# Kernel optimization log

Measured on AMD Instinct MI355X. Metric: run time of the kernel, lower is better.

## Reference

```python
import jax, jax.numpy as jnp
import numpy as np

B, S, D, H = 2, 2048, 1024, 16
DH = D // H  # dim per head (dim_singl_head)
SCALE = 0.02


def layer_norm(x, g, b, eps=1e-5):
    m = jnp.mean(x, axis=-1, keepdims=True)
    v = jnp.mean((x - m) ** 2, axis=-1, keepdims=True)
    return (x - m) / jnp.sqrt(v + eps) * g + b


def setup_inputs() -> dict:
    key = jax.random.key(0)
    ks = jax.random.split(key, 12)
    return {
        "query": jax.random.normal(ks[0], (B, S, D), jnp.float32),
        "key": jax.random.normal(ks[1], (B, S, D), jnp.float32),
        "value": jax.random.normal(ks[2], (B, S, D), jnp.float32),
        "mask": jax.random.randint(ks[3], (B, S), 0, 2).astype(jnp.int32),
        "Wq": jax.random.normal(ks[4], (D, D), jnp.float32) * SCALE,
        "bq": jnp.zeros((D,), jnp.float32),
        "Wk": jax.random.normal(ks[5], (D, D), jnp.float32) * SCALE,
        "bk": jnp.zeros((D,), jnp.float32),
        "Wv": jax.random.normal(ks[6], (D, D), jnp.float32) * SCALE,
        "bv": jnp.zeros((D,), jnp.float32),
        "g_att": jnp.ones((DH,), jnp.float32),
        "b_att": jnp.zeros((DH,), jnp.float32),
        "Wres": jax.random.normal(ks[7], (D, D), jnp.float32) * SCALE,
        "bres": jnp.zeros((D,), jnp.float32),
        "g_out": jnp.ones((D,), jnp.float32),
        "b_out": jnp.zeros((D,), jnp.float32),
    }


def reference(query, key, value, mask, Wq, bq, Wk, bk, Wv, bv,
              g_att, b_att, Wres, bres, g_out, b_out):
    # split heads: torch's split(dh,-1)+cat(dim=0) == [H,B,S,dh] layout
    def heads(x):
        return x.reshape(B, S, H, DH).transpose(2, 0, 1, 3)  # [H,B,S,dh]

    q = heads(query @ Wq + bq)
    k = heads(key @ Wk + bk)
    v = heads(value @ Wv + bv)

    # additive mask: (1-mask)*-1e9, broadcast [1,B,1,Sk]
    madd = (1.0 - mask.astype(q.dtype))[None, :, None, :] * -1e9

    scores = jnp.einsum('hbqd,hbkd->hbqk', q, k) / np.float32(np.sqrt(DH))
    w = jax.nn.softmax(scores + madd, axis=-1)
    out = jnp.einsum('hbqk,hbkd->hbqd', w, v)

    out = out + q                         # residual_att
    out = layer_norm(out, g_att, b_att)   # per-head LayerNorm on dh

    # concat heads back: [H,B,S,dh] -> [B,S,H*dh]
    out = out.transpose(1, 2, 0, 3).reshape(B, S, D)

    out = out + jnp.tanh(out @ Wres + bres)  # residual_out branch
    out = layer_norm(out, g_out, b_out)      # norm_out
    return jnp.tanh(out)                     # final activation
```

## Files before the change

### kernel.cpp

```cpp
#include <hip/hip_runtime.h>
#include <cstdint>
#include <cstddef>

#define BB 2
#define SS 2048
#define DD 1024
#define HH 16
#define DHH 64
#define MROWS (BB*SS)

typedef short short8 __attribute__((ext_vector_type(8)));
typedef short short4v __attribute__((ext_vector_type(4)));
typedef float floatx4 __attribute__((ext_vector_type(4)));
typedef unsigned int uint2v __attribute__((ext_vector_type(2)));

#define GAS __attribute__((address_space(1)))
#define LAS __attribute__((address_space(3)))

__device__ __forceinline__ float4 ld4(const float* p) { return *(const float4*)p; }

__device__ __forceinline__ short f2bf(float x) {
    unsigned u = __builtin_bit_cast(unsigned, x);
    unsigned r = (u + 0x7fffu + ((u >> 16) & 1u)) >> 16;
    return (short)r;
}

__device__ __forceinline__ unsigned cvtpk(float lo, float hi) {
    unsigned r;
    asm("v_cvt_pk_bf16_f32 %0, %1, %2" : "=v"(r) : "v"(lo), "v"(hi));
    return r;
}

__device__ __forceinline__ void gl_lds16(const short* g, short* l) {
    __builtin_amdgcn_global_load_lds((const GAS unsigned int*)g,
                                     (LAS unsigned int*)l, 16, 0, 0);
}

__global__ __launch_bounds__(256) void convert_kernel(
    const float* __restrict__ s0, const float* __restrict__ s1, const float* __restrict__ s2,
    short* __restrict__ d0, short* __restrict__ d1, short* __restrict__ d2)
{
    const float* s; short* d;
    if (blockIdx.z == 0)      { s = s0; d = d0; }
    else if (blockIdx.z == 1) { s = s1; d = d1; }
    else                      { s = s2; d = d2; }
    size_t idx = ((size_t)blockIdx.x * 256 + threadIdx.x) * 8;
    float4 a = ld4(s + idx);
    float4 b = ld4(s + idx + 4);
    short8 p;
    p[0] = f2bf(a.x); p[1] = f2bf(a.y); p[2] = f2bf(a.z); p[3] = f2bf(a.w);
    p[4] = f2bf(b.x); p[5] = f2bf(b.y); p[6] = f2bf(b.z); p[7] = f2bf(b.w);
    *(short8*)(d + idx) = p;
}

__global__ __launch_bounds__(256) void transpose_w_kernel(
    const float* __restrict__ W0, const float* __restrict__ W1,
    const float* __restrict__ W2, const float* __restrict__ W3,
    short* __restrict__ T0, short* __restrict__ T1,
    short* __restrict__ T2, short* __restrict__ T3)
{
    const float* W; short* T;
    if (blockIdx.z == 0)      { W = W0; T = T0; }
    else if (blockIdx.z == 1) { W = W1; T = T1; }
    else if (blockIdx.z == 2) { W = W2; T = T2; }
    else                      { W = W3; T = T3; }

    __shared__ short tile[64 * 72];
    const int t  = threadIdx.x;
    const int k0 = blockIdx.x * 64, n0 = blockIdx.y * 64;
#pragma unroll
    for (int i = 0; i < 4; i++) {
        int flat = i * 256 + t;
        int row = flat >> 4;
        int c4  = (flat & 15) * 4;
        float4 v = ld4(W + (size_t)(k0 + row) * DD + n0 + c4);
        tile[(c4 + 0) * 72 + row] = f2bf(v.x);
        tile[(c4 + 1) * 72 + row] = f2bf(v.y);
        tile[(c4 + 2) * 72 + row] = f2bf(v.z);
        tile[(c4 + 3) * 72 + row] = f2bf(v.w);
    }
    __syncthreads();
#pragma unroll
    for (int i = 0; i < 4; i++) {
        int flat = i * 256 + t;
        int nrow = flat >> 4;
        int kc   = (flat & 15) * 4;
        short4v pk = *(short4v*)&tile[nrow * 72 + kc];
        *(short4v*)(T + (size_t)(n0 + nrow) * DD + k0 + kc) = pk;
    }
}

__global__ __launch_bounds__(256) void gemm_bf16_kernel(
    const short* __restrict__ A0, const short* __restrict__ A1, const short* __restrict__ A2,
    const short* __restrict__ Bt0, const short* __restrict__ Bt1, const short* __restrict__ Bt2,
    const float* __restrict__ b0, const float* __restrict__ b1, const float* __restrict__ b2,
    float* __restrict__ Cf0, float* __restrict__ Cf1, float* __restrict__ Cf2,
    short* __restrict__ Cb0, short* __restrict__ Cb1, short* __restrict__ Cb2,
    short* __restrict__ Ct0, short* __restrict__ Ct1, short* __restrict__ Ct2,
    float cs0, float cs1, float cs2)
{
    const short* A; const short* Bt; const float* bias;
    float* Cf; short* Cb; short* Ct; float cbs;
    if (blockIdx.z == 0)      { A = A0; Bt = Bt0; bias = b0; Cf = Cf0; Cb = Cb0; Ct = Ct0; cbs = cs0; }
    else if (blockIdx.z == 1) { A = A1; Bt = Bt1; bias = b1; Cf = Cf1; Cb = Cb1; Ct = Ct1; cbs = cs1; }
    else                      { A = A2; Bt = Bt2; bias = b2; Cf = Cf2; Cb = Cb2; Ct = Ct2; cbs = cs2; }

    __shared__ __align__(16) short As[128 * 32];
    __shared__ __align__(16) short Bs[128 * 32];

    const int tid  = threadIdx.x;
    const int lane = tid & 63;
    const int wave = tid >> 6;
    const int quad = lane >> 4;
    const int l15  = lane & 15;
    const int m0 = blockIdx.y * 128;
    const int n0 = blockIdx.x * 128;
    const int wr = (wave >> 1) * 64;
    const int wc = (wave & 1) * 64;

    floatx4 acc[4][4];
#pragma unroll
    for (int mt = 0; mt < 4; mt++)
#pragma unroll
        for (int nt = 0; nt < 4; nt++) acc[mt][nt] = (floatx4)0.0f;

    for (int k0 = 0; k0 < DD; k0 += 32) {
        __syncthreads();
#pragma unroll
        for (int j = 0; j < 2; j++) {
            int chunk = j * 256 + tid;
            int row = chunk >> 2;
            int ch  = chunk & 3;
            gl_lds16(A  + (size_t)(m0 + row) * DD + k0 + ch * 8, &As[chunk * 8]);
            gl_lds16(Bt + (size_t)(n0 + row) * DD + k0 + ch * 8, &Bs[chunk * 8]);
        }
        __syncthreads();

        short8 af[4], bf[4];
#pragma unroll
        for (int mt = 0; mt < 4; mt++)
            af[mt] = *(const short8*)&As[(wr + mt * 16 + l15) * 32 + quad * 8];
#pragma unroll
        for (int nt = 0; nt < 4; nt++)
            bf[nt] = *(const short8*)&Bs[(wc + nt * 16 + l15) * 32 + quad * 8];
#pragma unroll
        for (int mt = 0; mt < 4; mt++)
#pragma unroll
            for (int nt = 0; nt < 4; nt++)
                acc[mt][nt] = __builtin_amdgcn_mfma_f32_16x16x32_bf16(af[mt], bf[nt], acc[mt][nt], 0, 0, 0);
    }

    float biasv[4];
#pragma unroll
    for (int nt = 0; nt < 4; nt++) biasv[nt] = bias[n0 + wc + nt * 16 + l15];

    if (Cf || Cb) {
#pragma unroll
        for (int mt = 0; mt < 4; mt++)
#pragma unroll
            for (int r = 0; r < 4; r++) {
                const int m = m0 + wr + mt * 16 + quad * 4 + r;
                const size_t rowb = (size_t)m * DD + n0 + wc;
#pragma unroll
                for (int nt = 0; nt < 4; nt++) {
                    float v = acc[mt][nt][r] + biasv[nt];
                    if (Cf) Cf[rowb + nt * 16 + l15] = v;
                    if (Cb) Cb[rowb + nt * 16 + l15] = f2bf(v * cbs);
                }
            }
    }
    if (Ct) {
#pragma unroll
        for (int mt = 0; mt < 4; mt++) {
            const int mbase = m0 + wr + mt * 16 + quad * 4;
            const int bb = mbase >> 11;
            const int s0 = mbase & 2047;
#pragma unroll
            for (int nt = 0; nt < 4; nt++) {
                const int c = n0 + wc + nt * 16 + l15;
                short4v pk;
#pragma unroll
                for (int r = 0; r < 4; r++) pk[r] = f2bf(acc[mt][nt][r] + biasv[nt]);
                *(short4v*)(Ct + ((size_t)(bb * 1024 + c)) * SS + s0) = pk;
            }
        }
    }
}

__global__ __launch_bounds__(256, 2) void attn_mfma_kernel(
    const short* __restrict__ Qb, const short* __restrict__ Kb, const short* __restrict__ Vt,
    const float* __restrict__ Qf, const int* __restrict__ mask,
    const float* __restrict__ g_att, const float* __restrict__ b_att,
    float* __restrict__ X, short* __restrict__ Xb)
{
    const int tid  = threadIdx.x;
    const int lane = tid & 63;
    const int wave = tid >> 6;
    const int quad = lane >> 4;
    const int l15  = lane & 15;

    const int h  = blockIdx.y;
    const int b  = blockIdx.z;
    const int q0 = blockIdx.x * 128;
    const int bS = b * SS;

    __shared__ __align__(16) short Ks[2 * 64 * 72];
    __shared__ __align__(16) short Vs[2 * 64 * 72];
    __shared__ __align__(16) short Ps[4 * 32 * 68];
    __shared__ float smadd[2 * 64];

    short8 qf[2][2];
#pragma unroll
    for (int mt = 0; mt < 2; mt++)
#pragma unroll
        for (int s = 0; s < 2; s++)
            qf[mt][s] = *(const short8*)(Qb +
                (size_t)(bS + q0 + wave * 32 + mt * 16 + l15) * DD + h * 64 + s * 32 + quad * 8);

    floatx4 o[2][4];
#pragma unroll
    for (int mt = 0; mt < 2; mt++)
#pragma unroll
        for (int nt = 0; nt < 4; nt++) o[mt][nt] = (floatx4)0.0f;
    float lsum[2] = {0.0f, 0.0f};

    const int srow = tid >> 3;
    const int sch  = tid & 7;

    short8 kreg[2], vreg[2];
    float mreg;
    {
#pragma unroll
        for (int i = 0; i < 2; i++) {
            int row = srow + i * 32;
            kreg[i] = *(const short8*)(Kb + (size_t)(bS + row) * DD + h * 64 + sch * 8);
            vreg[i] = *(const short8*)(Vt + (size_t)(b * 1024 + h * 64 + row) * SS + sch * 8);
        }
        mreg = (tid < 64) ? (float)mask[bS + tid] : 0.0f;
    }

    for (int kt = 0; kt < SS / 64; kt++) {
        const int bufo = (kt & 1) * (64 * 72);
#pragma unroll
        for (int i = 0; i < 2; i++) {
            int row = srow + i * 32;
            *(short8*)&Ks[bufo + row * 72 + sch * 8] = kreg[i];
            *(short8*)&Vs[bufo + row * 72 + sch * 8] = vreg[i];
        }
        if (tid < 64) smadd[(kt & 1) * 64 + tid] = (1.0f - mreg) * -1e9f;

        if (kt < SS / 64 - 1) {
            const int k0n = (kt + 1) * 64;
#pragma unroll
            for (int i = 0; i < 2; i++) {
                int row = srow + i * 32;
                kreg[i] = *(const short8*)(Kb + (size_t)(bS + k0n + row) * DD + h * 64 + sch * 8);
                vreg[i] = *(const short8*)(Vt + (size_t)(b * 1024 + h * 64 + row) * SS + k0n + sch * 8);
            }
            mreg = (tid < 64) ? (float)mask[bS + k0n + tid] : 0.0f;
        }

        __builtin_amdgcn_s_waitcnt(0xC07F);
        __builtin_amdgcn_s_barrier();

#pragma unroll
        for (int nt = 0; nt < 4; nt++) {
            const float4 mrow = *(const float4*)&smadd[(kt & 1) * 64 + nt * 16 + quad * 4];
#pragma unroll
            for (int mt = 0; mt < 2; mt++) {
                floatx4 acc = (floatx4)0.0f;
#pragma unroll
                for (int s = 0; s < 2; s++) {
                    short8 kf = *(const short8*)&Ks[bufo + (nt * 16 + l15) * 72 + s * 32 + quad * 8];
                    acc = __builtin_amdgcn_mfma_f32_16x16x32_bf16(kf, qf[mt][s], acc, 0, 0, 0);
                }
                float p0 = __builtin_exp2f(acc[0] + mrow.x);
                float p1 = __builtin_exp2f(acc[1] + mrow.y);
                float p2 = __builtin_exp2f(acc[2] + mrow.z);
                float p3 = __builtin_exp2f(acc[3] + mrow.w);
                lsum[mt] += (p0 + p1) + (p2 + p3);
                unsigned w0 = cvtpk(p0, p1);
                unsigned w1 = cvtpk(p2, p3);
                *(uint2v*)&Ps[wave * 2176 + (mt * 16 + l15) * 68 + nt * 16 + quad * 4]
                    = (uint2v){w0, w1};
            }
        }

#pragma unroll
        for (int s = 0; s < 2; s++) {
            short8 pa[2];
#pragma unroll
            for (int mt = 0; mt < 2; mt++)
                pa[mt] = *(const short8*)&Ps[wave * 2176 + (mt * 16 + l15) * 68 + s * 32 + quad * 8];
#pragma unroll
            for (int nt = 0; nt < 4; nt++) {
                short8 vb = *(const short8*)&Vs[bufo + (nt * 16 + l15) * 72 + s * 32 + quad * 8];
#pragma unroll
                for (int mt = 0; mt < 2; mt++)
                    o[mt][nt] = __builtin_amdgcn_mfma_f32_16x16x32_bf16(pa[mt], vb, o[mt][nt], 0, 0, 0);
            }
        }
    }

#pragma unroll
    for (int mt = 0; mt < 2; mt++) {
        lsum[mt] += __shfl_xor(lsum[mt], 16);
        lsum[mt] += __shfl_xor(lsum[mt], 32);
    }
    float rlq[2][4];
#pragma unroll
    for (int mt = 0; mt < 2; mt++)
#pragma unroll
        for (int r = 0; r < 4; r++)
            rlq[mt][r] = 1.0f / __shfl(lsum[mt], (lane & 48) | (quad * 4 + r));

    float gvv[4], bvv[4];
#pragma unroll
    for (int nt = 0; nt < 4; nt++) { gvv[nt] = g_att[nt * 16 + l15]; bvv[nt] = b_att[nt * 16 + l15]; }

#pragma unroll
    for (int mt = 0; mt < 2; mt++) {
        float x[4][4];
        float sum[4] = {0.f, 0.f, 0.f, 0.f};
#pragma unroll
        for (int r = 0; r < 4; r++) {
            const float rl = rlq[mt][r];
            const int row = q0 + wave * 32 + mt * 16 + quad * 4 + r;
            const size_t base = (size_t)(bS + row) * DD + h * 64;
#pragma unroll
            for (int nt = 0; nt < 4; nt++) {
                float xv = o[mt][nt][r] * rl + Qf[base + nt * 16 + l15];
                x[nt][r] = xv;
                sum[r] += xv;
            }
        }
#pragma unroll
        for (int r = 0; r < 4; r++)
#pragma unroll
            for (int off = 1; off < 16; off <<= 1) sum[r] += __shfl_xor(sum[r], off);

        float vsum[4] = {0.f, 0.f, 0.f, 0.f}, mu[4];
#pragma unroll
        for (int r = 0; r < 4; r++) {
            mu[r] = sum[r] * (1.0f / 64.0f);
#pragma unroll
            for (int nt = 0; nt < 4; nt++) { float d = x[nt][r] - mu[r]; vsum[r] += d * d; }
        }
#pragma unroll
        for (int r = 0; r < 4; r++) {
#pragma unroll
            for (int off = 1; off < 16; off <<= 1) vsum[r] += __shfl_xor(vsum[r], off);
            float rstd = rsqrtf(vsum[r] * (1.0f / 64.0f) + 1e-5f);
            const int row = q0 + wave * 32 + mt * 16 + quad * 4 + r;
            const size_t base = (size_t)(bS + row) * DD + h * 64;
#pragma unroll
            for (int nt = 0; nt < 4; nt++) {
                float yv = (x[nt][r] - mu[r]) * rstd * gvv[nt] + bvv[nt];
                X[base + nt * 16 + l15] = yv;
                Xb[base + nt * 16 + l15] = f2bf(yv);
            }
        }
    }
}

__global__ __launch_bounds__(256) void lnout_kernel(
    const float* __restrict__ X, const float* __restrict__ Y,
    const float* __restrict__ g, const float* __restrict__ bcoef,
    float* __restrict__ out)
{
    const int r = blockIdx.x;
    const int t = threadIdx.x;
    const size_t base = (size_t)r * DD + (t << 2);
    float4 x = ld4(X + base);
    float4 y = ld4(Y + base);
    float4 z;
    z.x = x.x + tanhf(y.x);
    z.y = x.y + tanhf(y.y);
    z.z = x.z + tanhf(y.z);
    z.w = x.w + tanhf(y.w);

    __shared__ float red[4];
    __shared__ float stats[2];
    const int w = t >> 6;

    float sv = z.x + z.y + z.z + z.w;
#pragma unroll
    for (int off = 32; off > 0; off >>= 1) sv += __shfl_down(sv, off);
    if ((t & 63) == 0) red[w] = sv;
    __syncthreads();
    if (t == 0) stats[0] = (red[0] + red[1] + red[2] + red[3]) * (1.0f / 1024.0f);
    __syncthreads();
    const float mu = stats[0];

    float4 d;
    d.x = z.x - mu; d.y = z.y - mu; d.z = z.z - mu; d.w = z.w - mu;
    float s2 = d.x * d.x + d.y * d.y + d.z * d.z + d.w * d.w;
#pragma unroll
    for (int off = 32; off > 0; off >>= 1) s2 += __shfl_down(s2, off);
    if ((t & 63) == 0) red[w] = s2;
    __syncthreads();
    if (t == 0) stats[1] = rsqrtf((red[0] + red[1] + red[2] + red[3]) * (1.0f / 1024.0f) + 1e-5f);
    __syncthreads();
    const float rstd = stats[1];

    float4 gv = ld4(g + (t << 2));
    float4 bv = ld4(bcoef + (t << 2));
    float4 o;
    o.x = tanhf(d.x * rstd * gv.x + bv.x);
    o.y = tanhf(d.y * rstd * gv.y + bv.y);
    o.z = tanhf(d.z * rstd * gv.z + bv.z);
    o.w = tanhf(d.w * rstd * gv.w + bv.w);
    *(float4*)(out + base) = o;
}

extern "C" void kernel_launch(void* const* d_in, const int* in_sizes, int n_in,
                              void* d_out, int out_size, void* d_ws, size_t ws_size,
                              hipStream_t stream)
{
    const float* query = (const float*)d_in[0];
    const float* key   = (const float*)d_in[1];
    const float* value = (const float*)d_in[2];
    const int*   mask  = (const int*)  d_in[3];
    const float* Wq    = (const float*)d_in[4];
    const float* bq    = (const float*)d_in[5];
    const float* Wk    = (const float*)d_in[6];
    const float* bk    = (const float*)d_in[7];
    const float* Wv    = (const float*)d_in[8];
    const float* bv    = (const float*)d_in[9];
    const float* g_att = (const float*)d_in[10];
    const float* b_att = (const float*)d_in[11];
    const float* Wres  = (const float*)d_in[12];
    const float* bres  = (const float*)d_in[13];
    const float* g_out = (const float*)d_in[14];
    const float* b_out = (const float*)d_in[15];

    const size_t MAT = (size_t)MROWS * DD;
    float* fws = (float*)d_ws;
    float* Qw = fws;
    float* Xw = fws + MAT;
    short* Qb = (short*)(fws + 2 * MAT);
    short* Kb = Qb + MAT;
    short* Vt = Kb + MAT;
    short* qbf = Vt + MAT;
    short* kbf = qbf + MAT;
    short* vbf = kbf + MAT;
    short* Wtq = vbf + MAT;
    short* Wtk = Wtq + DD * DD;
    short* Wtv = Wtk + DD * DD;
    short* Wtr = Wtv + DD * DD;
    short* Xb = qbf;
    float* Yw = (float*)kbf;

    convert_kernel<<<dim3(MAT / 2048, 1, 3), 256, 0, stream>>>(
        query, key, value, qbf, kbf, vbf);

    transpose_w_kernel<<<dim3(16, 16, 4), 256, 0, stream>>>(
        Wq, Wk, Wv, Wres, Wtq, Wtk, Wtv, Wtr);

    gemm_bf16_kernel<<<dim3(8, 32, 3), 256, 0, stream>>>(
        qbf, kbf, vbf, Wtq, Wtk, Wtv, bq, bk, bv,
        Qw, nullptr, nullptr,
        Qb, Kb, nullptr,
        nullptr, nullptr, Vt,
        0.180336884f, 1.0f, 1.0f);

    attn_mfma_kernel<<<dim3(SS / 128, HH, BB), 256, 0, stream>>>(
        Qb, Kb, Vt, Qw, mask, g_att, b_att, Xw, Xb);

    gemm_bf16_kernel<<<dim3(8, 32, 1), 256, 0, stream>>>(
        Xb, Xb, Xb, Wtr, Wtr, Wtr, bres, bres, bres,
        Yw, Yw, Yw, nullptr, nullptr, nullptr, nullptr, nullptr, nullptr,
        1.0f, 1.0f, 1.0f);

    lnout_kernel<<<MROWS, 256, 0, stream>>>(Xw, Yw, g_out, b_out, (float*)d_out);
}
```

Measured before the change: 290.0 us.

## Split attention block across 8 waves of 16 query rows each

The attention kernel now launches 512 threads per block, and each wave handles 16 query rows instead of 32. The per-wave Q fragments, output accumulators and P staging buffer shrink, and each thread loads one K/V row chunk per tile instead of two. This is meant to raise wave-level parallelism and latency hiding and to cut register pressure, with a launch bound of 4 blocks per CU. In exchange, each K/V tile held in shared memory is reused by fewer rows per wave, and there are more waves taking part in every barrier.

```diff
diff --git a/kernel.cpp b/kernel.cpp
--- a/kernel.cpp
+++ b/kernel.cpp
@@ -187,7 +187,7 @@
     }
 }
 
-__global__ __launch_bounds__(256, 2) void attn_mfma_kernel(
+__global__ __launch_bounds__(512, 4) void attn_mfma_kernel(
     const short* __restrict__ Qb, const short* __restrict__ Kb, const short* __restrict__ Vt,
     const float* __restrict__ Qf, const int* __restrict__ mask,
     const float* __restrict__ g_att, const float* __restrict__ b_att,
@@ -206,57 +206,41 @@
 
     __shared__ __align__(16) short Ks[2 * 64 * 72];
     __shared__ __align__(16) short Vs[2 * 64 * 72];
-    __shared__ __align__(16) short Ps[4 * 32 * 68];
+    __shared__ __align__(16) short Ps[8 * 16 * 68];
     __shared__ float smadd[2 * 64];
 
-    short8 qf[2][2];
-#pragma unroll
-    for (int mt = 0; mt < 2; mt++)
-#pragma unroll
-        for (int s = 0; s < 2; s++)
-            qf[mt][s] = *(const short8*)(Qb +
-                (size_t)(bS + q0 + wave * 32 + mt * 16 + l15) * DD + h * 64 + s * 32 + quad * 8);
-
-    floatx4 o[2][4];
-#pragma unroll
-    for (int mt = 0; mt < 2; mt++)
-#pragma unroll
-        for (int nt = 0; nt < 4; nt++) o[mt][nt] = (floatx4)0.0f;
-    float lsum[2] = {0.0f, 0.0f};
+    short8 qf[2];
+#pragma unroll
+    for (int s = 0; s < 2; s++)
+        qf[s] = *(const short8*)(Qb +
+            (size_t)(bS + q0 + wave * 16 + l15) * DD + h * 64 + s * 32 + quad * 8);
+
+    floatx4 o[4];
+#pragma unroll
+    for (int nt = 0; nt < 4; nt++) o[nt] = (floatx4)0.0f;
+    float lsum = 0.0f;
 
     const int srow = tid >> 3;
     const int sch  = tid & 7;
 
-    short8 kreg[2], vreg[2];
+    short8 kreg, vreg;
     float mreg;
     {
-#pragma unroll
-        for (int i = 0; i < 2; i++) {
-            int row = srow + i * 32;
-            kreg[i] = *(const short8*)(Kb + (size_t)(bS + row) * DD + h * 64 + sch * 8);
-            vreg[i] = *(const short8*)(Vt + (size_t)(b * 1024 + h * 64 + row) * SS + sch * 8);
-        }
+        kreg = *(const short8*)(Kb + (size_t)(bS + srow) * DD + h * 64 + sch * 8);
+        vreg = *(const short8*)(Vt + (size_t)(b * 1024 + h * 64 + srow) * SS + sch * 8);
         mreg = (tid < 64) ? (float)mask[bS + tid] : 0.0f;
     }
 
     for (int kt = 0; kt < SS / 64; kt++) {
         const int bufo = (kt & 1) * (64 * 72);
-#pragma unroll
-        for (int i = 0; i < 2; i++) {
-            int row = srow + i * 32;
-            *(short8*)&Ks[bufo + row * 72 + sch * 8] = kreg[i];
-            *(short8*)&Vs[bufo + row * 72 + sch * 8] = vreg[i];
-        }
+        *(short8*)&Ks[bufo + srow * 72 + sch * 8] = kreg;
+        *(short8*)&Vs[bufo + srow * 72 + sch * 8] = vreg;
         if (tid < 64) smadd[(kt & 1) * 64 + tid] = (1.0f - mreg) * -1e9f;
 
         if (kt < SS / 64 - 1) {
             const int k0n = (kt + 1) * 64;
-#pragma unroll
-            for (int i = 0; i < 2; i++) {
-                int row = srow + i * 32;
-                kreg[i] = *(const short8*)(Kb + (size_t)(bS + k0n + row) * DD + h * 64 + sch * 8);
-                vreg[i] = *(const short8*)(Vt + (size_t)(b * 1024 + h * 64 + row) * SS + k0n + sch * 8);
-            }
+            kreg = *(const short8*)(Kb + (size_t)(bS + k0n + srow) * DD + h * 64 + sch * 8);
+            vreg = *(const short8*)(Vt + (size_t)(b * 1024 + h * 64 + srow) * SS + k0n + sch * 8);
             mreg = (tid < 64) ? (float)mask[bS + k0n + tid] : 0.0f;
         }
 
@@ -266,99 +250,82 @@
 #pragma unroll
         for (int nt = 0; nt < 4; nt++) {
             const float4 mrow = *(const float4*)&smadd[(kt & 1) * 64 + nt * 16 + quad * 4];
-#pragma unroll
-            for (int mt = 0; mt < 2; mt++) {
-                floatx4 acc = (floatx4)0.0f;
-#pragma unroll
-                for (int s = 0; s < 2; s++) {
-                    short8 kf = *(const short8*)&Ks[bufo + (nt * 16 + l15) * 72 + s * 32 + quad * 8];
-                    acc = __builtin_amdgcn_mfma_f32_16x16x32_bf16(kf, qf[mt][s], acc, 0, 0, 0);
-                }
-                float p0 = __builtin_exp2f(acc[0] + mrow.x);
-                float p1 = __builtin_exp2f(acc[1] + mrow.y);
-                float p2 = __builtin_exp2f(acc[2] + mrow.z);
-                float p3 = __builtin_exp2f(acc[3] + mrow.w);
-                lsum[mt] += (p0 + p1) + (p2 + p3);
-                unsigned w0 = cvtpk(p0, p1);
-                unsigned w1 = cvtpk(p2, p3);
-                *(uint2v*)&Ps[wave * 2176 + (mt * 16 + l15) * 68 + nt * 16 + quad * 4]
-                    = (uint2v){w0, w1};
+            floatx4 acc = (floatx4)0.0f;
+#pragma unroll
+            for (int s = 0; s < 2; s++) {
+                short8 kf = *(const short8*)&Ks[bufo + (nt * 16 + l15) * 72 + s * 32 + quad * 8];
+                acc = __builtin_amdgcn_mfma_f32_16x16x32_bf16(kf, qf[s], acc, 0, 0, 0);
             }
+            float p0 = __builtin_exp2f(acc[0] + mrow.x);
+            float p1 = __builtin_exp2f(acc[1] + mrow.y);
+            float p2 = __builtin_exp2f(acc[2] + mrow.z);
+            float p3 = __builtin_exp2f(acc[3] + mrow.w);
+            lsum += (p0 + p1) + (p2 + p3);
+            unsigned w0 = cvtpk(p0, p1);
+            unsigned w1 = cvtpk(p2, p3);
+            *(uint2v*)&Ps[wave * 1088 + l15 * 68 + nt * 16 + quad * 4] = (uint2v){w0, w1};
         }
 
 #pragma unroll
         for (int s = 0; s < 2; s++) {
-            short8 pa[2];
-#pragma unroll
-            for (int mt = 0; mt < 2; mt++)
-                pa[mt] = *(const short8*)&Ps[wave * 2176 + (mt * 16 + l15) * 68 + s * 32 + quad * 8];
+            short8 pa = *(const short8*)&Ps[wave * 1088 + l15 * 68 + s * 32 + quad * 8];
 #pragma unroll
             for (int nt = 0; nt < 4; nt++) {
                 short8 vb = *(const short8*)&Vs[bufo + (nt * 16 + l15) * 72 + s * 32 + quad * 8];
-#pragma unroll
-                for (int mt = 0; mt < 2; mt++)
-                    o[mt][nt] = __builtin_amdgcn_mfma_f32_16x16x32_bf16(pa[mt], vb, o[mt][nt], 0, 0, 0);
+                o[nt] = __builtin_amdgcn_mfma_f32_16x16x32_bf16(pa, vb, o[nt], 0, 0, 0);
             }
         }
     }
 
-#pragma unroll
-    for (int mt = 0; mt < 2; mt++) {
-        lsum[mt] += __shfl_xor(lsum[mt], 16);
-        lsum[mt] += __shfl_xor(lsum[mt], 32);
-    }
-    float rlq[2][4];
-#pragma unroll
-    for (int mt = 0; mt < 2; mt++)
-#pragma unroll
-        for (int r = 0; r < 4; r++)
-            rlq[mt][r] = 1.0f / __shfl(lsum[mt], (lane & 48) | (quad * 4 + r));
+    lsum += __shfl_xor(lsum, 16);
+    lsum += __shfl_xor(lsum, 32);
+    float rlq[4];
+#pragma unroll
+    for (int r = 0; r < 4; r++)
+        rlq[r] = 1.0f / __shfl(lsum, (lane & 48) | (quad * 4 + r));
 
     float gvv[4], bvv[4];
 #pragma unroll
     for (int nt = 0; nt < 4; nt++) { gvv[nt] = g_att[nt * 16 + l15]; bvv[nt] = b_att[nt * 16 + l15]; }
 
-#pragma unroll
-    for (int mt = 0; mt < 2; mt++) {
-        float x[4][4];
-        float sum[4] = {0.f, 0.f, 0.f, 0.f};
-#pragma unroll
-        for (int r = 0; r < 4; r++) {
-            const float rl = rlq[mt][r];
-            const int row = q0 + wave * 32 + mt * 16 + quad * 4 + r;
-            const size_t base = (size_t)(bS + row) * DD + h * 64;
-#pragma unroll
-            for (int nt = 0; nt < 4; nt++) {
-                float xv = o[mt][nt][r] * rl + Qf[base + nt * 16 + l15];
-                x[nt][r] = xv;
-                sum[r] += xv;
-            }
-        }
-#pragma unroll
-        for (int r = 0; r < 4; r++)
-#pragma unroll
-            for (int off = 1; off < 16; off <<= 1) sum[r] += __shfl_xor(sum[r], off);
-
-        float vsum[4] = {0.f, 0.f, 0.f, 0.f}, mu[4];
-#pragma unroll
-        for (int r = 0; r < 4; r++) {
-            mu[r] = sum[r] * (1.0f / 64.0f);
-#pragma unroll
-            for (int nt = 0; nt < 4; nt++) { float d = x[nt][r] - mu[r]; vsum[r] += d * d; }
-        }
-#pragma unroll
-        for (int r = 0; r < 4; r++) {
-#pragma unroll
-            for (int off = 1; off < 16; off <<= 1) vsum[r] += __shfl_xor(vsum[r], off);
-            float rstd = rsqrtf(vsum[r] * (1.0f / 64.0f) + 1e-5f);
-            const int row = q0 + wave * 32 + mt * 16 + quad * 4 + r;
-            const size_t base = (size_t)(bS + row) * DD + h * 64;
-#pragma unroll
-            for (int nt = 0; nt < 4; nt++) {
-                float yv = (x[nt][r] - mu[r]) * rstd * gvv[nt] + bvv[nt];
-                X[base + nt * 16 + l15] = yv;
-                Xb[base + nt * 16 + l15] = f2bf(yv);
-            }
+    float x[4][4];
+    float sum[4] = {0.f, 0.f, 0.f, 0.f};
+#pragma unroll
+    for (int r = 0; r < 4; r++) {
+        const float rl = rlq[r];
+        const int row = q0 + wave * 16 + quad * 4 + r;
+        const size_t base = (size_t)(bS + row) * DD + h * 64;
+#pragma unroll
+        for (int nt = 0; nt < 4; nt++) {
+            float xv = o[nt][r] * rl + Qf[base + nt * 16 + l15];
+            x[nt][r] = xv;
+            sum[r] += xv;
+        }
+    }
+#pragma unroll
+    for (int r = 0; r < 4; r++)
+#pragma unroll
+        for (int off = 1; off < 16; off <<= 1) sum[r] += __shfl_xor(sum[r], off);
+
+    float vsum[4] = {0.f, 0.f, 0.f, 0.f}, mu[4];
+#pragma unroll
+    for (int r = 0; r < 4; r++) {
+        mu[r] = sum[r] * (1.0f / 64.0f);
+#pragma unroll
+        for (int nt = 0; nt < 4; nt++) { float d = x[nt][r] - mu[r]; vsum[r] += d * d; }
+    }
+#pragma unroll
+    for (int r = 0; r < 4; r++) {
+#pragma unroll
+        for (int off = 1; off < 16; off <<= 1) vsum[r] += __shfl_xor(vsum[r], off);
+        float rstd = rsqrtf(vsum[r] * (1.0f / 64.0f) + 1e-5f);
+        const int row = q0 + wave * 16 + quad * 4 + r;
+        const size_t base = (size_t)(bS + row) * DD + h * 64;
+#pragma unroll
+        for (int nt = 0; nt < 4; nt++) {
+            float yv = (x[nt][r] - mu[r]) * rstd * gvv[nt] + bvv[nt];
+            X[base + nt * 16 + l15] = yv;
+            Xb[base + nt * 16 + l15] = f2bf(yv);
         }
     }
 }
@@ -464,7 +431,7 @@
         nullptr, nullptr, Vt,
         0.180336884f, 1.0f, 1.0f);
 
-    attn_mfma_kernel<<<dim3(SS / 128, HH, BB), 256, 0, stream>>>(
+    attn_mfma_kernel<<<dim3(SS / 128, HH, BB), 512, 0, stream>>>(
         Qb, Kb, Vt, Qw, mask, g_att, b_att, Xw, Xb);
 
     gemm_bf16_kernel<<<dim3(8, 32, 1), 256, 0, stream>>>(
```

Measured after the change: 286.1 us. Within noise of the previous version (-1.4%).
